# Kernel tuning notes

Hardware: AMD Instinct MI355X
Metric: run time of the kernel (lower is better)

Reference implementation:

```python
import jax, jax.numpy as jnp
import numpy as np

HIDDEN_DIM = 128
NUM_HEADS = 4
B, S = 16, 1024
NEG = -1e9
EPS = 1e-5


def setup_inputs() -> dict:
    key = jax.random.key(0)
    ks = jax.random.split(key, 6)
    D, H = HIDDEN_DIM, NUM_HEADS
    x = jax.random.normal(ks[0], (B, S, D), dtype=jnp.float32)
    edge_type_matrix = jax.random.randint(ks[1], (S, S), 0, 5, dtype=jnp.int64)
    scale = 0.02
    W_in = jax.random.normal(ks[2], (H, 3 * D, D), dtype=jnp.float32) * scale   # per-head in_proj_weight
    b_in = jax.random.normal(ks[3], (H, 3 * D), dtype=jnp.float32) * scale      # per-head in_proj_bias
    W_out = jax.random.normal(ks[4], (H, D, D), dtype=jnp.float32) * scale      # per-head out_proj.weight
    b_out = jax.random.normal(ks[5], (H, D), dtype=jnp.float32) * scale         # per-head out_proj.bias
    return {"x": x, "edge_type_matrix": edge_type_matrix,
            "W_in": W_in, "b_in": b_in, "W_out": W_out, "b_out": b_out}


def reference(x, edge_type_matrix, W_in, b_in, W_out, b_out):
    Bx, Sx, D = x.shape
    H = W_in.shape[0]
    # F.layer_norm(x, x.size()[1:]): normalize jointly over (S, D), no affine
    mu = jnp.mean(x, axis=(1, 2), keepdims=True)
    var = jnp.mean(jnp.square(x - mu), axis=(1, 2), keepdims=True)
    xn = (x - mu) / jnp.sqrt(var + EPS)
    # all heads' qkv in one contraction: [b,h,s,3D]
    qkv = jnp.einsum('bsd,hed->bhse', xn, W_in) + b_in[None, :, None, :]
    q, k, v = jnp.split(qkv, 3, axis=-1)                      # each [b,h,s,D]
    scores = jnp.einsum('bhsd,bhtd->bhst', q, k) / jnp.sqrt(jnp.float32(D))
    # additive mask per head: 0 where edge_type == head_id(1..H), else -1e9
    head_ids = jnp.arange(1, H + 1, dtype=edge_type_matrix.dtype)
    mask = jnp.where(edge_type_matrix[None, :, :] == head_ids[:, None, None],
                     jnp.float32(0.0), jnp.float32(NEG))       # [h,s,s]
    attn = jax.nn.softmax(scores + mask[None], axis=-1)
    ctx = jnp.einsum('bhst,bhtd->bhsd', attn, v)
    # torch out_proj: ctx @ W.T + b
    out_h = jnp.einsum('bhsd,hed->bhse', ctx, W_out) + b_out[None, :, None, :]
    # dropout p=0.05 is identity in eval mode; concat heads on feature dim
    out = jnp.transpose(out_h, (0, 2, 1, 3)).reshape(Bx, Sx, H * D)
    return out


if __name__ == '__main__':
    inp = setup_inputs()
    y = reference(**inp)
    print(y.shape)
```

## Files before the change

kernel.cpp:

```cpp
#include <hip/hip_runtime.h>
#include <math.h>

static constexpr int Dh = 128;
static constexpr int NH = 4;
static constexpr int NB = 16;
static constexpr int SS = 1024;
static constexpr float NEGF = -1e9f;
static constexpr float SCALE = 0.08838834764831843f;
static constexpr float LOG2E = 1.4426950408889634f;

typedef short s16x8 __attribute__((ext_vector_type(8)));
typedef short s16x4 __attribute__((ext_vector_type(4)));
typedef float f32x4 __attribute__((ext_vector_type(4)));

#define MFMA32(a, b, c) __builtin_amdgcn_mfma_f32_16x16x32_bf16(a, b, c, 0, 0, 0)
#define MFMA16(a, b, c) __builtin_amdgcn_mfma_f32_16x16x16bf16_1k(a, b, c, 0, 0, 0)

__device__ inline ushort f2bf(float f) {
    union { float f; unsigned u; } v; v.f = f;
    unsigned r = v.u + 0x7FFFu + ((v.u >> 16) & 1u);
    return (ushort)(r >> 16);
}

__global__ __launch_bounds__(256) void ln_mask_kernel(const float* __restrict__ x,
                                                      float* __restrict__ part,
                                                      const int* __restrict__ edge,
                                                      unsigned long long* __restrict__ mbit,
                                                      const float* __restrict__ w_in,
                                                      const float* __restrict__ w_out,
                                                      ushort* __restrict__ wb,
                                                      ushort* __restrict__ wob) {
    const int b = blockIdx.x >> 4, p = blockIdx.x & 15;
    const int tid = threadIdx.x;
    const float4* xb4 = (const float4*)(x + (size_t)b * SS * Dh) + p * 2048;
    float s = 0.f, ss = 0.f;
    for (int i = tid; i < 2048; i += 256) {
        float4 v = xb4[i];
        s  += v.x + v.y + v.z + v.w;
        ss += v.x * v.x + v.y * v.y + v.z * v.z + v.w * v.w;
    }
    __shared__ float r1[256], r2[256];
    r1[tid] = s; r2[tid] = ss;
    __syncthreads();
    for (int off = 128; off > 0; off >>= 1) {
        if (tid < off) { r1[tid] += r1[tid + off]; r2[tid] += r2[tid + off]; }
        __syncthreads();
    }
    if (tid == 0) { part[blockIdx.x * 2] = r1[0]; part[blockIdx.x * 2 + 1] = r2[0]; }

    if (blockIdx.x < 64) {
        const int idx = blockIdx.x * 256 + tid;
        const int sr = idx >> 4, w = idx & 15;
        const int4* ep = (const int4*)(edge + (size_t)sr * SS + w * 64);
        unsigned long long m0 = 0, m1 = 0, m2 = 0, m3 = 0;
        #pragma unroll
        for (int j = 0; j < 16; ++j) {
            int4 e = ep[j];
            const int base = j * 4;
            m0 |= (e.x == 1) ? (1ull << (base + 0)) : 0ull;
            m1 |= (e.x == 2) ? (1ull << (base + 0)) : 0ull;
            m2 |= (e.x == 3) ? (1ull << (base + 0)) : 0ull;
            m3 |= (e.x == 4) ? (1ull << (base + 0)) : 0ull;
            m0 |= (e.y == 1) ? (1ull << (base + 1)) : 0ull;
            m1 |= (e.y == 2) ? (1ull << (base + 1)) : 0ull;
            m2 |= (e.y == 3) ? (1ull << (base + 1)) : 0ull;
            m3 |= (e.y == 4) ? (1ull << (base + 1)) : 0ull;
            m0 |= (e.z == 1) ? (1ull << (base + 2)) : 0ull;
            m1 |= (e.z == 2) ? (1ull << (base + 2)) : 0ull;
            m2 |= (e.z == 3) ? (1ull << (base + 2)) : 0ull;
            m3 |= (e.z == 4) ? (1ull << (base + 2)) : 0ull;
            m0 |= (e.w == 1) ? (1ull << (base + 3)) : 0ull;
            m1 |= (e.w == 2) ? (1ull << (base + 3)) : 0ull;
            m2 |= (e.w == 3) ? (1ull << (base + 3)) : 0ull;
            m3 |= (e.w == 4) ? (1ull << (base + 3)) : 0ull;
        }
        mbit[((size_t)0 * SS + sr) * 16 + w] = m0;
        mbit[((size_t)1 * SS + sr) * 16 + w] = m1;
        mbit[((size_t)2 * SS + sr) * 16 + w] = m2;
        mbit[((size_t)3 * SS + sr) * 16 + w] = m3;
    } else if (blockIdx.x < 160) {
        const int slot = (blockIdx.x - 64) * 256 + tid;
        const float4* sp = (const float4*)w_in + (size_t)slot * 2;
        float4 a = sp[0], c = sp[1];
        s16x8 pk;
        pk[0] = (short)f2bf(a.x); pk[1] = (short)f2bf(a.y);
        pk[2] = (short)f2bf(a.z); pk[3] = (short)f2bf(a.w);
        pk[4] = (short)f2bf(c.x); pk[5] = (short)f2bf(c.y);
        pk[6] = (short)f2bf(c.z); pk[7] = (short)f2bf(c.w);
        *(s16x8*)(wb + (size_t)slot * 8) = pk;
    } else if (blockIdx.x < 192) {
        const int slot = (blockIdx.x - 160) * 256 + tid;
        const float4* sp = (const float4*)w_out + (size_t)slot * 2;
        float4 a = sp[0], c = sp[1];
        s16x8 pk;
        pk[0] = (short)f2bf(a.x); pk[1] = (short)f2bf(a.y);
        pk[2] = (short)f2bf(a.z); pk[3] = (short)f2bf(a.w);
        pk[4] = (short)f2bf(c.x); pk[5] = (short)f2bf(c.y);
        pk[6] = (short)f2bf(c.z); pk[7] = (short)f2bf(c.w);
        *(s16x8*)(wob + (size_t)slot * 8) = pk;
    }
}

__global__ __launch_bounds__(256) void xcast_kernel(const float* __restrict__ x,
                                                    const float* __restrict__ part,
                                                    ushort* __restrict__ xb) {
    const int b = blockIdx.x >> 6;
    float s = 0.f, ss = 0.f;
    #pragma unroll
    for (int p = 0; p < 16; ++p) { s += part[(b * 16 + p) * 2]; ss += part[(b * 16 + p) * 2 + 1]; }
    const float invN = 1.0f / (float)(SS * Dh);
    const float mu = s * invN;
    const float rstd = 1.0f / sqrtf(ss * invN - mu * mu + 1e-5f);
    const size_t base = ((size_t)blockIdx.x * 256 + threadIdx.x) * 8;
    float4 v0 = *(const float4*)(x + base);
    float4 v1 = *(const float4*)(x + base + 4);
    s16x8 pk;
    pk[0] = (short)f2bf((v0.x - mu) * rstd); pk[1] = (short)f2bf((v0.y - mu) * rstd);
    pk[2] = (short)f2bf((v0.z - mu) * rstd); pk[3] = (short)f2bf((v0.w - mu) * rstd);
    pk[4] = (short)f2bf((v1.x - mu) * rstd); pk[5] = (short)f2bf((v1.y - mu) * rstd);
    pk[6] = (short)f2bf((v1.z - mu) * rstd); pk[7] = (short)f2bf((v1.w - mu) * rstd);
    *(s16x8*)(xb + base) = pk;
}

__global__ __launch_bounds__(256) void qkv_mfma_kernel(const ushort* __restrict__ xb,
                                                       const ushort* __restrict__ wb,
                                                       const float* __restrict__ bias,
                                                       ushort* __restrict__ qo,
                                                       ushort* __restrict__ ko,
                                                       ushort* __restrict__ vto) {
    __shared__ ushort smem[2 * 128 * 72];
    ushort* As = smem;
    ushort* Bs = smem + 128 * 72;
    ushort* Rs = smem;
    const int tid = threadIdx.x, wave = tid >> 6, lane = tid & 63;
    const int lrow = lane & 15, quad = lane >> 4;
    const int wm = wave & 1, wn = wave >> 1;
    const int col0 = blockIdx.x * 128;
    const int row0 = blockIdx.y * 128;
    const int bb = row0 >> 10;

    f32x4 acc[4][4];
    #pragma unroll
    for (int mi = 0; mi < 4; ++mi)
        #pragma unroll
        for (int ni = 0; ni < 4; ++ni) acc[mi][ni] = (f32x4){0.f, 0.f, 0.f, 0.f};

    for (int kk = 0; kk < 128; kk += 64) {
        if (kk) __syncthreads();
        #pragma unroll
        for (int p = 0; p < 4; ++p) {
            int slot = p * 256 + tid;
            int r = slot >> 3, c8 = (slot & 7) * 8;
            *(s16x8*)&As[r * 72 + c8] = *(const s16x8*)(xb + (size_t)(row0 + r) * Dh + kk + c8);
            *(s16x8*)&Bs[r * 72 + c8] = *(const s16x8*)(wb + (size_t)(col0 + r) * Dh + kk + c8);
        }
        __syncthreads();
        #pragma unroll
        for (int kc = 0; kc < 2; ++kc) {
            s16x8 af[4], bf[4];
            #pragma unroll
            for (int mi = 0; mi < 4; ++mi)
                af[mi] = *(const s16x8*)&As[(wm * 64 + 16 * mi + lrow) * 72 + kc * 32 + quad * 8];
            #pragma unroll
            for (int ni = 0; ni < 4; ++ni)
                bf[ni] = *(const s16x8*)&Bs[(wn * 64 + 16 * ni + lrow) * 72 + kc * 32 + quad * 8];
            #pragma unroll
            for (int mi = 0; mi < 4; ++mi)
                #pragma unroll
                for (int ni = 0; ni < 4; ++ni)
                    acc[mi][ni] = MFMA32(af[mi], bf[ni], acc[mi][ni]);
        }
    }

    const int seg = col0 % 384, typ = seg >> 7, h = col0 / 384;
    const size_t bh = (size_t)bb * NH + h;
    const int sl_blk = row0 & 1023;
    float bia[4];
    #pragma unroll
    for (int ni = 0; ni < 4; ++ni) bia[ni] = bias[col0 + wn * 64 + 16 * ni + lrow];
    const float sc = (typ == 0) ? SCALE * LOG2E : 1.f;

    __syncthreads();
    if (typ < 2) {
        #pragma unroll
        for (int mi = 0; mi < 4; ++mi)
            #pragma unroll
            for (int ni = 0; ni < 4; ++ni)
                #pragma unroll
                for (int reg = 0; reg < 4; ++reg)
                    Rs[(wm * 64 + 16 * mi + quad * 4 + reg) * 136 + wn * 64 + 16 * ni + lrow]
                        = f2bf((acc[mi][ni][reg] + bia[ni]) * sc);
    } else {
        #pragma unroll
        for (int mi = 0; mi < 4; ++mi)
            #pragma unroll
            for (int ni = 0; ni < 4; ++ni) {
                ushort4 pk;
                pk.x = f2bf(acc[mi][ni][0] + bia[ni]);
                pk.y = f2bf(acc[mi][ni][1] + bia[ni]);
                pk.z = f2bf(acc[mi][ni][2] + bia[ni]);
                pk.w = f2bf(acc[mi][ni][3] + bia[ni]);
                *(ushort4*)&Rs[(wn * 64 + 16 * ni + lrow) * 136 + wm * 64 + 16 * mi + quad * 4] = pk;
            }
    }
    __syncthreads();

    ushort* dstb;
    int pitch;
    if (typ == 0)      { dstb = qo  + bh * SS * 128 + (size_t)sl_blk * 128; pitch = 128; }
    else if (typ == 1) { dstb = ko  + bh * SS * 128 + (size_t)sl_blk * 128; pitch = 128; }
    else               { dstb = vto + bh * (size_t)128 * SS + sl_blk;       pitch = SS;  }
    #pragma unroll
    for (int p = 0; p < 8; ++p) {
        int slot = p * 256 + tid;
        int r = slot >> 4, c8 = (slot & 15) * 8;
        *(s16x8*)&dstb[(size_t)r * pitch + c8] = *(const s16x8*)&Rs[r * 136 + c8];
    }
}

static constexpr int VT_LD = 72;
static constexpr int HALF = 64 * 128 + 128 * VT_LD;

__global__ __launch_bounds__(256, 2) void attn_fused_kernel(const ushort* __restrict__ qg_,
                                                            const ushort* __restrict__ kg_,
                                                            const ushort* __restrict__ vg_,
                                                            const unsigned long long* __restrict__ mbit,
                                                            const ushort* __restrict__ wob,
                                                            const float* __restrict__ bo,
                                                            float* __restrict__ out) {
    const int bhi = blockIdx.x, qt = blockIdx.y;
    const int b = bhi >> 2, h = bhi & 3;
    const int s0 = qt * 128;
    const int tid = threadIdx.x;
    const int wave = tid >> 6, lane = tid & 63;
    const int lrow = lane & 15, quad = lane >> 4;

    __shared__ ushort smem[2 * HALF];

    const size_t bh = (size_t)(b * NH + h);
    const ushort* qg = qg_ + bh * SS * 128;
    const ushort* kg = kg_ + bh * SS * 128;
    const ushort* vg = vg_ + bh * (size_t)128 * SS;
    const unsigned long long* mrow0 = mbit + ((size_t)h * SS + (s0 + 32 * wave + lrow)) * 16;
    const unsigned long long* mrow1 = mrow0 + 16 * 16;

    s16x8 qf[2][4];
    #pragma unroll
    for (int g = 0; g < 2; ++g) {
        const ushort* qr = qg + (size_t)(s0 + 32 * wave + 16 * g + lrow) * 128 + quad * 8;
        #pragma unroll
        for (int kc = 0; kc < 4; ++kc) qf[g][kc] = *(const s16x8*)(qr + kc * 32);
    }

    s16x8 kreg[4], vreg[4];
    #pragma unroll
    for (int p = 0; p < 4; ++p) {
        int slot = p * 256 + tid;
        int r = slot >> 4, c = (slot & 15) * 8;
        kreg[p] = *(const s16x8*)(kg + (size_t)r * 128 + c);
    }
    #pragma unroll
    for (int p = 0; p < 4; ++p) {
        int slot = p * 256 + tid;
        int r = slot >> 3, c = (slot & 7) * 8;
        vreg[p] = *(const s16x8*)(vg + (size_t)r * SS + c);
    }
    {
        ushort* Ks0 = smem;
        ushort* Vt0 = smem + 64 * 128;
        #pragma unroll
        for (int p = 0; p < 4; ++p) {
            int slot = p * 256 + tid;
            int r = slot >> 4, c = (slot & 15) * 8;
            *(s16x8*)&Ks0[r * 128 + (c ^ ((r & 7) << 3))] = kreg[p];
        }
        #pragma unroll
        for (int p = 0; p < 4; ++p) {
            int slot = p * 256 + tid;
            int r = slot >> 3, c = (slot & 7) * 8;
            *(s16x8*)&Vt0[r * VT_LD + c] = vreg[p];
        }
    }

    f32x4 oacc[2][8];
    #pragma unroll
    for (int g = 0; g < 2; ++g)
        #pragma unroll
        for (int nb = 0; nb < 8; ++nb) oacc[g][nb] = (f32x4){0.f, 0.f, 0.f, 0.f};
    float m_run[2] = {-INFINITY, -INFINITY};
    float l_run[2] = {0.f, 0.f};

    for (int kt = 0; kt < 16; ++kt) {
        const unsigned long long mw0 = mrow0[kt];
        const unsigned long long mw1 = mrow1[kt];
        const ushort* Ksc = smem + (kt & 1) * HALF;
        const ushort* Vtc = Ksc + 64 * 128;

        __syncthreads();

        if (kt < 15) {
            const int t1 = (kt + 1) * 64;
            #pragma unroll
            for (int p = 0; p < 4; ++p) {
                int slot = p * 256 + tid;
                int r = slot >> 4, c = (slot & 15) * 8;
                kreg[p] = *(const s16x8*)(kg + (size_t)(t1 + r) * 128 + c);
            }
            #pragma unroll
            for (int p = 0; p < 4; ++p) {
                int slot = p * 256 + tid;
                int r = slot >> 3, c = (slot & 7) * 8;
                vreg[p] = *(const s16x8*)(vg + (size_t)r * SS + t1 + c);
            }
        }

        f32x4 sacc[2][4];
        #pragma unroll
        for (int g = 0; g < 2; ++g)
            #pragma unroll
            for (int cb = 0; cb < 4; ++cb) sacc[g][cb] = (f32x4){0.f, 0.f, 0.f, 0.f};
        __builtin_amdgcn_s_setprio(1);
        #pragma unroll
        for (int cb = 0; cb < 4; ++cb) {
            s16x8 kf[4];
            const int krow = 16 * cb + lrow;
            #pragma unroll
            for (int kc = 0; kc < 4; ++kc)
                kf[kc] = *(const s16x8*)&Ksc[krow * 128 + ((kc * 32 + quad * 8) ^ ((lrow & 7) << 3))];
            #pragma unroll
            for (int kc = 0; kc < 4; ++kc) {
                sacc[0][cb] = MFMA32(kf[kc], qf[0][kc], sacc[0][cb]);
                sacc[1][cb] = MFMA32(kf[kc], qf[1][kc], sacc[1][cb]);
            }
        }
        __builtin_amdgcn_s_setprio(0);

        s16x4 pf[2][4];
        #pragma unroll
        for (int g = 0; g < 2; ++g) {
            const unsigned long long mw = g ? mw1 : mw0;
            float sv[4][4];
            float tm = -INFINITY;
            #pragma unroll
            for (int cb = 0; cb < 4; ++cb) {
                unsigned nib = (unsigned)(mw >> (16 * cb + quad * 4)) & 0xFu;
                #pragma unroll
                for (int r = 0; r < 4; ++r) {
                    sv[cb][r] = (nib & (1u << r)) ? sacc[g][cb][r] : NEGF;
                    tm = fmaxf(tm, sv[cb][r]);
                }
            }
            tm = fmaxf(tm, __shfl_xor(tm, 16));
            tm = fmaxf(tm, __shfl_xor(tm, 32));
            float mn = m_run[g];
            if (!__all(tm <= mn + 12.f)) {
                mn = fmaxf(mn, tm);
                float al = __builtin_amdgcn_exp2f(m_run[g] - mn);
                l_run[g] *= al;
                #pragma unroll
                for (int nb = 0; nb < 8; ++nb)
                    #pragma unroll
                    for (int r = 0; r < 4; ++r) oacc[g][nb][r] *= al;
                m_run[g] = mn;
            }
            float rs = 0.f;
            #pragma unroll
            for (int cb = 0; cb < 4; ++cb) {
                float p0 = __builtin_amdgcn_exp2f(sv[cb][0] - mn);
                float p1 = __builtin_amdgcn_exp2f(sv[cb][1] - mn);
                float p2 = __builtin_amdgcn_exp2f(sv[cb][2] - mn);
                float p3 = __builtin_amdgcn_exp2f(sv[cb][3] - mn);
                rs += (p0 + p1) + (p2 + p3);
                s16x4 pk;
                pk[0] = (short)f2bf(p0); pk[1] = (short)f2bf(p1);
                pk[2] = (short)f2bf(p2); pk[3] = (short)f2bf(p3);
                pf[g][cb] = pk;
            }
            rs += __shfl_xor(rs, 16);
            rs += __shfl_xor(rs, 32);
            l_run[g] += rs;
        }

        __builtin_amdgcn_s_setprio(1);
        #pragma unroll
        for (int nb = 0; nb < 8; ++nb) {
            #pragma unroll
            for (int kb = 0; kb < 4; ++kb) {
                s16x4 vf = *(const s16x4*)&Vtc[(16 * nb + lrow) * VT_LD + kb * 16 + quad * 4];
                oacc[0][nb] = MFMA16(vf, pf[0][kb], oacc[0][nb]);
                oacc[1][nb] = MFMA16(vf, pf[1][kb], oacc[1][nb]);
            }
        }
        __builtin_amdgcn_s_setprio(0);

        if (kt < 15) {
            ushort* Ksn = smem + ((kt + 1) & 1) * HALF;
            ushort* Vtn = Ksn + 64 * 128;
            #pragma unroll
            for (int p = 0; p < 4; ++p) {
                int slot = p * 256 + tid;
                int r = slot >> 4, c = (slot & 15) * 8;
                *(s16x8*)&Ksn[r * 128 + (c ^ ((r & 7) << 3))] = kreg[p];
            }
            #pragma unroll
            for (int p = 0; p < 4; ++p) {
                int slot = p * 256 + tid;
                int r = slot >> 3, c = (slot & 7) * 8;
                *(s16x8*)&Vtn[r * VT_LD + c] = vreg[p];
            }
        }
    }

    s16x4 aO[2][8];
    #pragma unroll
    for (int g = 0; g < 2; ++g) {
        float inv = 1.0f / l_run[g];
        #pragma unroll
        for (int nb = 0; nb < 8; ++nb) {
            s16x4 pk;
            pk[0] = (short)f2bf(oacc[g][nb][0] * inv);
            pk[1] = (short)f2bf(oacc[g][nb][1] * inv);
            pk[2] = (short)f2bf(oacc[g][nb][2] * inv);
            pk[3] = (short)f2bf(oacc[g][nb][3] * inv);
            aO[g][nb] = pk;
        }
    }
    const ushort* wbh = wob + (size_t)h * Dh * Dh;
    const size_t orow0 = (size_t)b * SS + s0 + 32 * wave;
    #pragma unroll
    for (int eb = 0; eb < 8; ++eb) {
        float bia = bo[h * Dh + eb * 16 + lrow];
        f32x4 facc[2];
        facc[0] = (f32x4){0.f, 0.f, 0.f, 0.f};
        facc[1] = (f32x4){0.f, 0.f, 0.f, 0.f};
        const ushort* wr = wbh + (size_t)(eb * 16 + lrow) * Dh + quad * 4;
        #pragma unroll
        for (int nb = 0; nb < 8; ++nb) {
            s16x4 wf = *(const s16x4*)(wr + nb * 16);
            facc[0] = MFMA16(aO[0][nb], wf, facc[0]);
            facc[1] = MFMA16(aO[1][nb], wf, facc[1]);
        }
        #pragma unroll
        for (int g = 0; g < 2; ++g)
            #pragma unroll
            for (int reg = 0; reg < 4; ++reg) {
                size_t m = orow0 + 16 * g + quad * 4 + reg;
                out[m * (NH * Dh) + h * Dh + eb * 16 + lrow] = facc[g][reg] + bia;
            }
    }
}

extern "C" void kernel_launch(void* const* d_in, const int* in_sizes, int n_in,
                              void* d_out, int out_size, void* d_ws, size_t ws_size,
                              hipStream_t stream) {
    const float* x     = (const float*)d_in[0];
    const int*   edge  = (const int*)d_in[1];
    const float* w_in  = (const float*)d_in[2];
    const float* b_in  = (const float*)d_in[3];
    const float* w_out = (const float*)d_in[4];
    const float* b_out = (const float*)d_in[5];
    float* out = (float*)d_out;

    float* ws   = (float*)d_ws;
    float* part = ws;
    unsigned long long* mbit = (unsigned long long*)(ws + 1024);
    ushort* qo  = (ushort*)(mbit + (size_t)NH * SS * 16);
    const size_t QSZ = (size_t)NB * NH * SS * 128;
    ushort* ko  = qo + QSZ;
    ushort* vto = ko + QSZ;
    ushort* xb  = vto + QSZ;
    ushort* wb  = xb + (size_t)NB * SS * Dh;
    ushort* wob = wb + (size_t)NH * 3 * Dh * Dh;

    ln_mask_kernel<<<256, 256, 0, stream>>>(x, part, edge, mbit, w_in, w_out, wb, wob);
    xcast_kernel<<<1024, 256, 0, stream>>>(x, part, xb);
    qkv_mfma_kernel<<<dim3(12, 128), 256, 0, stream>>>(xb, wb, b_in, qo, ko, vto);
    attn_fused_kernel<<<dim3(NB * NH, SS / 128), 256, 0, stream>>>(qo, ko, vto, mbit, wob, b_out, out);
}
```

Measured before the change: 165.8 us.

## Split attention KV range across two wave groups with split-K softmax merge

Doubles the attention block to 512 threads, with two groups of four waves each processing half of the key/value sequence (8 tiles instead of 16). Partial online-softmax states are merged through shared memory, and each group then performs the output projection for one 16-row half. The change drops the register double-buffered LDS ping-pong in favour of a single buffer per group with two barriers per tile. It also removes the setprio hints and adds an XOR swizzle to the V tile. It aims to raise wave-level parallelism and occupancy on a grid of only 512 blocks, at the cost of more barriers, a merge step, and less load/compute overlap.

```diff
diff --git a/kernel.cpp b/kernel.cpp
--- a/kernel.cpp
+++ b/kernel.cpp
@@ -218,10 +218,11 @@
     }
 }
 
-static constexpr int VT_LD = 72;
-static constexpr int HALF = 64 * 128 + 128 * VT_LD;
-
-__global__ __launch_bounds__(256, 2) void attn_fused_kernel(const ushort* __restrict__ qg_,
+static constexpr int KBUF = 64 * 128;
+static constexpr int VBUF = 128 * 64;
+static constexpr int BUFU = KBUF + VBUF;
+
+__global__ __launch_bounds__(512, 4) void attn_fused_kernel(const ushort* __restrict__ qg_,
                                                             const ushort* __restrict__ kg_,
                                                             const ushort* __restrict__ vg_,
                                                             const unsigned long long* __restrict__ mbit,
@@ -233,21 +234,26 @@
     const int s0 = qt * 128;
     const int tid = threadIdx.x;
     const int wave = tid >> 6, lane = tid & 63;
+    const int wl = wave & 3;
+    const int kh = wave >> 2;
+    const int htid = tid & 255;
     const int lrow = lane & 15, quad = lane >> 4;
 
-    __shared__ ushort smem[2 * HALF];
+    __shared__ ushort smem[2 * BUFU];
+    ushort* Ks = smem + kh * BUFU;
+    ushort* Vt = smem + kh * BUFU + KBUF;
 
     const size_t bh = (size_t)(b * NH + h);
     const ushort* qg = qg_ + bh * SS * 128;
-    const ushort* kg = kg_ + bh * SS * 128;
-    const ushort* vg = vg_ + bh * (size_t)128 * SS;
-    const unsigned long long* mrow0 = mbit + ((size_t)h * SS + (s0 + 32 * wave + lrow)) * 16;
+    const ushort* kg = kg_ + bh * SS * 128 + (size_t)(kh * 512) * 128;
+    const ushort* vg = vg_ + bh * (size_t)128 * SS + kh * 512;
+    const unsigned long long* mrow0 = mbit + ((size_t)h * SS + (s0 + 32 * wl + lrow)) * 16 + kh * 8;
     const unsigned long long* mrow1 = mrow0 + 16 * 16;
 
     s16x8 qf[2][4];
     #pragma unroll
     for (int g = 0; g < 2; ++g) {
-        const ushort* qr = qg + (size_t)(s0 + 32 * wave + 16 * g + lrow) * 128 + quad * 8;
+        const ushort* qr = qg + (size_t)(s0 + 32 * wl + 16 * g + lrow) * 128 + quad * 8;
         #pragma unroll
         for (int kc = 0; kc < 4; ++kc) qf[g][kc] = *(const s16x8*)(qr + kc * 32);
     }
@@ -255,31 +261,15 @@
     s16x8 kreg[4], vreg[4];
     #pragma unroll
     for (int p = 0; p < 4; ++p) {
-        int slot = p * 256 + tid;
+        int slot = p * 256 + htid;
         int r = slot >> 4, c = (slot & 15) * 8;
         kreg[p] = *(const s16x8*)(kg + (size_t)r * 128 + c);
     }
     #pragma unroll
     for (int p = 0; p < 4; ++p) {
-        int slot = p * 256 + tid;
+        int slot = p * 256 + htid;
         int r = slot >> 3, c = (slot & 7) * 8;
         vreg[p] = *(const s16x8*)(vg + (size_t)r * SS + c);
-    }
-    {
-        ushort* Ks0 = smem;
-        ushort* Vt0 = smem + 64 * 128;
-        #pragma unroll
-        for (int p = 0; p < 4; ++p) {
-            int slot = p * 256 + tid;
-            int r = slot >> 4, c = (slot & 15) * 8;
-            *(s16x8*)&Ks0[r * 128 + (c ^ ((r & 7) << 3))] = kreg[p];
-        }
-        #pragma unroll
-        for (int p = 0; p < 4; ++p) {
-            int slot = p * 256 + tid;
-            int r = slot >> 3, c = (slot & 7) * 8;
-            *(s16x8*)&Vt0[r * VT_LD + c] = vreg[p];
-        }
     }
 
     f32x4 oacc[2][8];
@@ -290,25 +280,36 @@
     float m_run[2] = {-INFINITY, -INFINITY};
     float l_run[2] = {0.f, 0.f};
 
-    for (int kt = 0; kt < 16; ++kt) {
+    for (int kt = 0; kt < 8; ++kt) {
         const unsigned long long mw0 = mrow0[kt];
         const unsigned long long mw1 = mrow1[kt];
-        const ushort* Ksc = smem + (kt & 1) * HALF;
-        const ushort* Vtc = Ksc + 64 * 128;
 
         __syncthreads();
-
-        if (kt < 15) {
+        #pragma unroll
+        for (int p = 0; p < 4; ++p) {
+            int slot = p * 256 + htid;
+            int r = slot >> 4, c = (slot & 15) * 8;
+            *(s16x8*)&Ks[r * 128 + (c ^ ((r & 7) << 3))] = kreg[p];
+        }
+        #pragma unroll
+        for (int p = 0; p < 4; ++p) {
+            int slot = p * 256 + htid;
+            int r = slot >> 3, c = (slot & 7) * 8;
+            *(s16x8*)&Vt[r * 64 + (c ^ ((r & 7) << 3))] = vreg[p];
+        }
+        __syncthreads();
+
+        if (kt < 7) {
             const int t1 = (kt + 1) * 64;
             #pragma unroll
             for (int p = 0; p < 4; ++p) {
-                int slot = p * 256 + tid;
+                int slot = p * 256 + htid;
                 int r = slot >> 4, c = (slot & 15) * 8;
                 kreg[p] = *(const s16x8*)(kg + (size_t)(t1 + r) * 128 + c);
             }
             #pragma unroll
             for (int p = 0; p < 4; ++p) {
-                int slot = p * 256 + tid;
+                int slot = p * 256 + htid;
                 int r = slot >> 3, c = (slot & 7) * 8;
                 vreg[p] = *(const s16x8*)(vg + (size_t)r * SS + t1 + c);
             }
@@ -319,21 +320,19 @@
         for (int g = 0; g < 2; ++g)
             #pragma unroll
             for (int cb = 0; cb < 4; ++cb) sacc[g][cb] = (f32x4){0.f, 0.f, 0.f, 0.f};
-        __builtin_amdgcn_s_setprio(1);
         #pragma unroll
         for (int cb = 0; cb < 4; ++cb) {
             s16x8 kf[4];
             const int krow = 16 * cb + lrow;
             #pragma unroll
             for (int kc = 0; kc < 4; ++kc)
-                kf[kc] = *(const s16x8*)&Ksc[krow * 128 + ((kc * 32 + quad * 8) ^ ((lrow & 7) << 3))];
+                kf[kc] = *(const s16x8*)&Ks[krow * 128 + ((kc * 32 + quad * 8) ^ ((lrow & 7) << 3))];
             #pragma unroll
             for (int kc = 0; kc < 4; ++kc) {
                 sacc[0][cb] = MFMA32(kf[kc], qf[0][kc], sacc[0][cb]);
                 sacc[1][cb] = MFMA32(kf[kc], qf[1][kc], sacc[1][cb]);
             }
         }
-        __builtin_amdgcn_s_setprio(0);
 
         s16x4 pf[2][4];
         #pragma unroll
@@ -381,72 +380,93 @@
             l_run[g] += rs;
         }
 
-        __builtin_amdgcn_s_setprio(1);
         #pragma unroll
         for (int nb = 0; nb < 8; ++nb) {
+            const int vrow = 16 * nb + lrow;
             #pragma unroll
             for (int kb = 0; kb < 4; ++kb) {
-                s16x4 vf = *(const s16x4*)&Vtc[(16 * nb + lrow) * VT_LD + kb * 16 + quad * 4];
+                s16x4 vf = *(const s16x4*)&Vt[vrow * 64 + ((kb * 16 + quad * 4) ^ ((lrow & 7) << 3))];
                 oacc[0][nb] = MFMA16(vf, pf[0][kb], oacc[0][nb]);
                 oacc[1][nb] = MFMA16(vf, pf[1][kb], oacc[1][nb]);
             }
         }
-        __builtin_amdgcn_s_setprio(0);
-
-        if (kt < 15) {
-            ushort* Ksn = smem + ((kt + 1) & 1) * HALF;
-            ushort* Vtn = Ksn + 64 * 128;
-            #pragma unroll
-            for (int p = 0; p < 4; ++p) {
-                int slot = p * 256 + tid;
-                int r = slot >> 4, c = (slot & 15) * 8;
-                *(s16x8*)&Ksn[r * 128 + (c ^ ((r & 7) << 3))] = kreg[p];
-            }
-            #pragma unroll
-            for (int p = 0; p < 4; ++p) {
-                int slot = p * 256 + tid;
-                int r = slot >> 3, c = (slot & 7) * 8;
-                *(s16x8*)&Vtn[r * VT_LD + c] = vreg[p];
-            }
-        }
-    }
-
-    s16x4 aO[2][8];
-    #pragma unroll
-    for (int g = 0; g < 2; ++g) {
-        float inv = 1.0f / l_run[g];
+    }
+
+    float* ar = (float*)smem;
+    const int aslot = (wl * 64 + lane) * 35;
+    __syncthreads();
+    if (kh == 1) {
+        #pragma unroll
+        for (int nb = 0; nb < 8; ++nb)
+            #pragma unroll
+            for (int r = 0; r < 4; ++r) ar[aslot + nb * 4 + r] = oacc[0][nb][r];
+        ar[aslot + 32] = m_run[0];
+        ar[aslot + 33] = l_run[0];
+    }
+    __syncthreads();
+    if (kh == 0) {
+        float m1 = ar[aslot + 32], l1 = ar[aslot + 33];
+        float mN = fmaxf(m_run[0], m1);
+        float a0 = __builtin_amdgcn_exp2f(m_run[0] - mN);
+        float a1 = __builtin_amdgcn_exp2f(m1 - mN);
+        l_run[0] = l_run[0] * a0 + l1 * a1;
+        #pragma unroll
+        for (int nb = 0; nb < 8; ++nb)
+            #pragma unroll
+            for (int r = 0; r < 4; ++r)
+                oacc[0][nb][r] = oacc[0][nb][r] * a0 + ar[aslot + nb * 4 + r] * a1;
+        #pragma unroll
+        for (int nb = 0; nb < 8; ++nb)
+            #pragma unroll
+            for (int r = 0; r < 4; ++r) ar[aslot + nb * 4 + r] = oacc[1][nb][r];
+        ar[aslot + 32] = m_run[1];
+        ar[aslot + 33] = l_run[1];
+    }
+    __syncthreads();
+    if (kh == 1) {
+        float m0 = ar[aslot + 32], l0 = ar[aslot + 33];
+        float mN = fmaxf(m_run[1], m0);
+        float a1 = __builtin_amdgcn_exp2f(m_run[1] - mN);
+        float a0 = __builtin_amdgcn_exp2f(m0 - mN);
+        l_run[1] = l_run[1] * a1 + l0 * a0;
+        #pragma unroll
+        for (int nb = 0; nb < 8; ++nb)
+            #pragma unroll
+            for (int r = 0; r < 4; ++r)
+                oacc[1][nb][r] = oacc[1][nb][r] * a1 + ar[aslot + nb * 4 + r] * a0;
+    }
+
+    const int gsel = kh;
+    s16x4 aO[8];
+    {
+        float inv = 1.0f / l_run[gsel];
         #pragma unroll
         for (int nb = 0; nb < 8; ++nb) {
             s16x4 pk;
-            pk[0] = (short)f2bf(oacc[g][nb][0] * inv);
-            pk[1] = (short)f2bf(oacc[g][nb][1] * inv);
-            pk[2] = (short)f2bf(oacc[g][nb][2] * inv);
-            pk[3] = (short)f2bf(oacc[g][nb][3] * inv);
-            aO[g][nb] = pk;
+            pk[0] = (short)f2bf(oacc[gsel][nb][0] * inv);
+            pk[1] = (short)f2bf(oacc[gsel][nb][1] * inv);
+            pk[2] = (short)f2bf(oacc[gsel][nb][2] * inv);
+            pk[3] = (short)f2bf(oacc[gsel][nb][3] * inv);
+            aO[nb] = pk;
         }
     }
     const ushort* wbh = wob + (size_t)h * Dh * Dh;
-    const size_t orow0 = (size_t)b * SS + s0 + 32 * wave;
+    const size_t orow0 = (size_t)b * SS + s0 + 32 * wl + 16 * gsel;
     #pragma unroll
     for (int eb = 0; eb < 8; ++eb) {
         float bia = bo[h * Dh + eb * 16 + lrow];
-        f32x4 facc[2];
-        facc[0] = (f32x4){0.f, 0.f, 0.f, 0.f};
-        facc[1] = (f32x4){0.f, 0.f, 0.f, 0.f};
+        f32x4 facc = (f32x4){0.f, 0.f, 0.f, 0.f};
         const ushort* wr = wbh + (size_t)(eb * 16 + lrow) * Dh + quad * 4;
         #pragma unroll
         for (int nb = 0; nb < 8; ++nb) {
             s16x4 wf = *(const s16x4*)(wr + nb * 16);
-            facc[0] = MFMA16(aO[0][nb], wf, facc[0]);
-            facc[1] = MFMA16(aO[1][nb], wf, facc[1]);
-        }
-        #pragma unroll
-        for (int g = 0; g < 2; ++g)
-            #pragma unroll
-            for (int reg = 0; reg < 4; ++reg) {
-                size_t m = orow0 + 16 * g + quad * 4 + reg;
-                out[m * (NH * Dh) + h * Dh + eb * 16 + lrow] = facc[g][reg] + bia;
-            }
+            facc = MFMA16(aO[nb], wf, facc);
+        }
+        #pragma unroll
+        for (int reg = 0; reg < 4; ++reg) {
+            size_t m = orow0 + quad * 4 + reg;
+            out[m * (NH * Dh) + h * Dh + eb * 16 + lrow] = facc[reg] + bia;
+        }
     }
 }
 
@@ -475,5 +495,5 @@
     ln_mask_kernel<<<256, 256, 0, stream>>>(x, part, edge, mbit, w_in, w_out, wb, wob);
     xcast_kernel<<<1024, 256, 0, stream>>>(x, part, xb);
     qkv_mfma_kernel<<<dim3(12, 128), 256, 0, stream>>>(xb, wb, b_in, qo, ko, vto);
-    attn_fused_kernel<<<dim3(NB * NH, SS / 128), 256, 0, stream>>>(qo, ko, vto, mbit, wob, b_out, out);
-}
+    attn_fused_kernel<<<dim3(NB * NH, SS / 128), 512, 0, stream>>>(qo, ko, vto, mbit, wob, b_out, out);
+}
```

Result: slower. 609.4 us (+267.5%).
